# Performance work log

Measured on AMD Instinct MI355X. Metric: run time of the kernel, lower is better.

The kernel has to match this reference:

```python
import jax, jax.numpy as jnp
import numpy as np

B = 256
LSTM = 512
FEAT = 3 * 3 * 512 + 16 + 8  # 4632
N_ACT = 4
ACT_SHAPE = 64
NUM_STEPS = 20
CANVAS_IN = 6 * 32 * 32  # 6144
H1 = int(FEAT / (FEAT / LSTM) ** (1.0 / 3.0))  # 2223
H2 = int(FEAT / (FEAT / LSTM) ** (2.0 / 3.0))  # 1067


def setup_inputs() -> dict:
    key = jax.random.key(0)
    ks = jax.random.split(key, 32)

    def g(k, shape, scale=0.02):
        return jax.random.normal(k, shape, dtype=jnp.float32) * scale

    inp = {
        "actualCanvas": jax.random.normal(ks[0], (B, 3, 32, 32), dtype=jnp.float32),
        "objectiveCanvas": jax.random.normal(ks[1], (B, 3, 32, 32), dtype=jnp.float32),
        "last_action_end_position": jax.random.randint(ks[2], (B,), 0, ACT_SHAPE),
        "episode_percentage": jax.random.randint(ks[3], (B,), 0, NUM_STEPS),
        # feature extractor stub (flatten -> linear -> relu), output 4608
        "Wfe": g(ks[4], (4608, CANVAS_IN)), "bfe": jnp.zeros((4608,), jnp.float32),
        "emb_end": g(ks[5], (ACT_SHAPE, 16), 1.0),
        "emb_ep": g(ks[6], (NUM_STEPS, 8), 1.0),
        "W1": g(ks[7], (H1, FEAT)), "b1": jnp.zeros((H1,), jnp.float32),
        "W2": g(ks[8], (H2, H1)), "b2": jnp.zeros((H2,), jnp.float32),
        "W3": g(ks[9], (LSTM, H2)), "b3": jnp.zeros((LSTM,), jnp.float32),
        "W_ih": g(ks[10], (4 * LSTM, LSTM)), "W_hh": g(ks[11], (4 * LSTM, LSTM)),
        "b_ih": jnp.zeros((4 * LSTM,), jnp.float32), "b_hh": jnp.zeros((4 * LSTM,), jnp.float32),
        "Wd1": g(ks[12], (N_ACT, LSTM // 2, LSTM)), "bd1": jnp.zeros((N_ACT, LSTM // 2), jnp.float32),
        "Wd2": g(ks[13], (N_ACT, ACT_SHAPE, LSTM // 2)), "bd2": jnp.zeros((N_ACT, ACT_SHAPE), jnp.float32),
        "emb_dec": g(ks[14], (N_ACT, ACT_SHAPE, 16), 1.0),
        "Wout": g(ks[15], (LSTM, LSTM + 16)), "bout": jnp.zeros((LSTM,), jnp.float32),
    }
    return inp


def reference(actualCanvas, objectiveCanvas, last_action_end_position, episode_percentage,
              Wfe, bfe, emb_end, emb_ep, W1, b1, W2, b2, W3, b3,
              W_ih, W_hh, b_ih, b_hh, Wd1, bd1, Wd2, bd2, emb_dec, Wout, bout):
    # feature extractor on channel-concatenated canvases -> [B, 4608]
    x = jnp.concatenate([actualCanvas, objectiveCanvas], axis=1).reshape(B, -1)
    fv = jax.nn.relu(x @ Wfe.T + bfe)
    feats = jnp.concatenate([fv, emb_end[last_action_end_position], emb_ep[episode_percentage]], axis=1)
    # fc1->fc2->fc3 (dropout = eval mode / identity)
    h = jax.nn.relu(feats @ W1.T + b1)
    h = jax.nn.relu(h @ W2.T + b2)
    h = jax.nn.relu(h @ W3.T + b3)  # [B, LSTM]
    # single-step LSTM with zero initial state (first execution)
    gates = h @ W_ih.T + b_ih + b_hh  # h0 = 0 so recurrent matmul vanishes
    i, f, g_, o = jnp.split(gates, 4, axis=1)
    c = jax.nn.sigmoid(i) * jnp.tanh(g_)
    seed = jax.nn.sigmoid(o) * jnp.tanh(c)  # [B, LSTM]
    z = seed
    log_probabilities = jnp.zeros((B,), jnp.float32)
    entropy = jnp.float32(0.0)
    actions = []
    base_key = jax.random.key(42)
    for k in range(N_ACT):
        hm = jax.nn.relu(z @ Wd1[k].T + bd1[k])
        logits = hm @ Wd2[k].T + bd2[k]  # [B, ACT_SHAPE]
        logp = jax.nn.log_softmax(logits, axis=1)
        probs = jnp.exp(logp)
        entropy = entropy + jnp.sum(-probs * logp)
        act = jax.random.categorical(jax.random.fold_in(base_key, k), logits, axis=1)  # [B]
        actions.append(act)
        log_probabilities = log_probabilities + jnp.take_along_axis(logp, act[:, None], axis=1)[:, 0]
        emb_a = emb_dec[k][act]  # [B,16]
        z = jax.nn.relu(jnp.concatenate([z, emb_a], axis=1) @ Wout.T + bout)
    action = jnp.stack(actions, axis=1)  # [B, N_ACT]
    return action, entropy, log_probabilities
```

## Files before the change

### kernel.cpp

```cpp
#include <hip/hip_runtime.h>
#include <hip/hip_bf16.h>
#include <stdint.h>

#define B_SZ   256
#define LSTM_N 512
#define FEAT_N 4632
#define FV_N   4608
#define CIN_N  6144
#define HALF_CIN 3072
#define ACT_N  64
#define LDSW   72
#define LD_FEAT 4672
#define LD_ZEXT 576

typedef __attribute__((ext_vector_type(8))) short bf16x8;
typedef __attribute__((ext_vector_type(4))) float f32x4;

__device__ __forceinline__ short f2bf(float f) {
  uint32_t u = __float_as_uint(f);
  u += 0x7FFFu + ((u >> 16) & 1u);
  return (short)(u >> 16);
}
__device__ __forceinline__ float bf2f(short s) {
  return __uint_as_float(((uint32_t)(uint16_t)s) << 16);
}

__device__ __forceinline__ uint32_t rotl32(uint32_t x, int r) {
  return (x << r) | (x >> (32 - r));
}
__device__ __forceinline__ void threefry2x32(uint32_t k0, uint32_t k1,
                                             uint32_t x0, uint32_t x1,
                                             uint32_t& o0, uint32_t& o1) {
  uint32_t k2 = k0 ^ k1 ^ 0x1BD11BDAu;
  x0 += k0; x1 += k1;
  x0 += x1; x1 = rotl32(x1, 13); x1 ^= x0;
  x0 += x1; x1 = rotl32(x1, 15); x1 ^= x0;
  x0 += x1; x1 = rotl32(x1, 26); x1 ^= x0;
  x0 += x1; x1 = rotl32(x1,  6); x1 ^= x0;
  x0 += k1; x1 += k2 + 1u;
  x0 += x1; x1 = rotl32(x1, 17); x1 ^= x0;
  x0 += x1; x1 = rotl32(x1, 29); x1 ^= x0;
  x0 += x1; x1 = rotl32(x1, 16); x1 ^= x0;
  x0 += x1; x1 = rotl32(x1, 24); x1 ^= x0;
  x0 += k2; x1 += k0 + 2u;
  x0 += x1; x1 = rotl32(x1, 13); x1 ^= x0;
  x0 += x1; x1 = rotl32(x1, 15); x1 ^= x0;
  x0 += x1; x1 = rotl32(x1, 26); x1 ^= x0;
  x0 += x1; x1 = rotl32(x1,  6); x1 ^= x0;
  x0 += k0; x1 += k1 + 3u;
  x0 += x1; x1 = rotl32(x1, 17); x1 ^= x0;
  x0 += x1; x1 = rotl32(x1, 29); x1 ^= x0;
  x0 += x1; x1 = rotl32(x1, 16); x1 ^= x0;
  x0 += x1; x1 = rotl32(x1, 24); x1 ^= x0;
  x0 += k1; x1 += k2 + 4u;
  x0 += x1; x1 = rotl32(x1, 13); x1 ^= x0;
  x0 += x1; x1 = rotl32(x1, 15); x1 ^= x0;
  x0 += x1; x1 = rotl32(x1, 26); x1 ^= x0;
  x0 += x1; x1 = rotl32(x1,  6); x1 ^= x0;
  x0 += k2; x1 += k0 + 5u;
  o0 = x0; o1 = x1;
}

__global__ void concat_cvt_kernel(const float* __restrict__ act,
                                  const float* __restrict__ obj,
                                  short* __restrict__ xb) {
  int idx = blockIdx.x * 256 + threadIdx.x;
  if (idx >= B_SZ * 768) return;
  int row = idx / 768;
  int c8 = (idx - row * 768) * 8;
  const float* src = (c8 < HALF_CIN) ? (act + (size_t)row * HALF_CIN + c8)
                                     : (obj + (size_t)row * HALF_CIN + (c8 - HALF_CIN));
  float4 u = ((const float4*)src)[0];
  float4 v = ((const float4*)src)[1];
  bf16x8 r;
  r[0]=f2bf(u.x); r[1]=f2bf(u.y); r[2]=f2bf(u.z); r[3]=f2bf(u.w);
  r[4]=f2bf(v.x); r[5]=f2bf(v.y); r[6]=f2bf(v.z); r[7]=f2bf(v.w);
  *(bf16x8*)&xb[(size_t)row * CIN_N + c8] = r;
}

__global__ void fill_embs_kernel(const int* __restrict__ lastpos,
                                 const int* __restrict__ ep,
                                 const float* __restrict__ emb_end,
                                 const float* __restrict__ emb_ep,
                                 short* __restrict__ feats) {
  int b = blockIdx.x;
  int t = threadIdx.x;
  short* row = feats + (size_t)b * LD_FEAT;
  if (t < 16) {
    row[FV_N + t] = f2bf(emb_end[lastpos[b] * 16 + t]);
  } else if (t < 24) {
    row[FV_N + 16 + (t - 16)] = f2bf(emb_ep[ep[b] * 8 + (t - 16)]);
  } else {
    row[FV_N + t] = 0;
  }
}

__global__ __launch_bounds__(512) void gemm3_kernel(
    const short* __restrict__ A, int ldab,
    const float* __restrict__ W, int ldw,
    const float* __restrict__ bias1, const float* __restrict__ bias2,
    void* __restrict__ Cout, int ldc,
    short* __restrict__ P,
    int N, int K, int do_relu, int mode_f32, int kc, int nchunks) {
  __shared__ short Wlds[2][64 * LDSW];

  const int tid = threadIdx.x;
  const int w = tid >> 6, l = tid & 63, l15 = l & 15, lg = l >> 4;
  const int n0 = blockIdx.x * 64;
  const int Np = gridDim.x * 64;
  const int ks = blockIdx.y;
  const int kbeg = ks * kc;
  const int kend = (kbeg + kc < K) ? (kbeg + kc) : K;
  const int nk = (kend - kbeg + 63) >> 6;
  const bool wfast = ((ldw & 3) == 0);

  f32x4 acc[2][4];
#pragma unroll
  for (int i = 0; i < 2; ++i)
#pragma unroll
    for (int j = 0; j < 4; ++j) acc[i][j] = (f32x4){0.f, 0.f, 0.f, 0.f};

  const int wrow = tid >> 3, wq = tid & 7;

  auto loadW = [&](float4* dst, int k0) {
    int gn = n0 + wrow; if (gn >= N) gn = N - 1;
    int gk = k0 + (wq << 3);
    const float* p = W + (size_t)gn * ldw + gk;
    if (wfast && (k0 + 64 <= K)) {
      dst[0] = ((const float4*)p)[0];
      dst[1] = ((const float4*)p)[1];
    } else {
      float t[8];
#pragma unroll
      for (int j = 0; j < 8; ++j) t[j] = (gk + j < K) ? p[j] : 0.f;
      dst[0] = (float4){t[0], t[1], t[2], t[3]};
      dst[1] = (float4){t[4], t[5], t[6], t[7]};
    }
  };
  auto storeW = [&](const float4* src, int buf) {
    short4 s0, s1;
    s0.x = f2bf(src[0].x); s0.y = f2bf(src[0].y);
    s0.z = f2bf(src[0].z); s0.w = f2bf(src[0].w);
    s1.x = f2bf(src[1].x); s1.y = f2bf(src[1].y);
    s1.z = f2bf(src[1].z); s1.w = f2bf(src[1].w);
    short* q = &Wlds[buf][wrow * LDSW + (wq << 3)];
    *(short4*)q = s0;
    *(short4*)(q + 4) = s1;
  };
  auto loadA = [&](bf16x8* dst, int k0) {
#pragma unroll
    for (int mi = 0; mi < 2; ++mi)
#pragma unroll
      for (int kh = 0; kh < 2; ++kh) {
        int m = (w << 5) + (mi << 4) + l15;
        int kk = k0 + (kh << 5) + (lg << 3);
        dst[(mi << 1) + kh] = *(const bf16x8*)&A[(size_t)m * ldab + kk];
      }
  };

#define MFMA_STEP(ACUR, BUF)                                                        \
  {                                                                                 \
    _Pragma("unroll")                                                               \
    for (int nj = 0; nj < 4; ++nj) {                                                \
      const short* bp = &Wlds[BUF][((nj << 4) + l15) * LDSW + (lg << 3)];           \
      bf16x8 b0 = *(const bf16x8*)bp;                                               \
      bf16x8 b1 = *(const bf16x8*)(bp + 32);                                        \
      acc[0][nj] = __builtin_amdgcn_mfma_f32_16x16x32_bf16(ACUR[0], b0, acc[0][nj], 0, 0, 0); \
      acc[1][nj] = __builtin_amdgcn_mfma_f32_16x16x32_bf16(ACUR[2], b0, acc[1][nj], 0, 0, 0); \
      acc[0][nj] = __builtin_amdgcn_mfma_f32_16x16x32_bf16(ACUR[1], b1, acc[0][nj], 0, 0, 0); \
      acc[1][nj] = __builtin_amdgcn_mfma_f32_16x16x32_bf16(ACUR[3], b1, acc[1][nj], 0, 0, 0); \
    }                                                                               \
  }

#define STEP(KT, ACUR, ANXT, WCUR, WNXT, BUF, BUFN)          \
  {                                                          \
    if ((KT) + 1 < nk) loadA(ANXT, kbeg + (((KT) + 1) << 6));\
    if ((KT) + 2 < nk) loadW(WCUR, kbeg + (((KT) + 2) << 6));\
    MFMA_STEP(ACUR, BUF);                                    \
    if ((KT) + 1 < nk) { storeW(WNXT, BUFN); __syncthreads(); } \
  }

  bf16x8 a0[4], a1[4];
  float4 wr0[2], wr1[2];

  loadW(wr0, kbeg);
  loadA(a0, kbeg);
  storeW(wr0, 0);
  if (nk > 1) loadW(wr1, kbeg + 64);
  __syncthreads();

  for (int kt = 0; kt < nk; kt += 2) {
    STEP(kt, a0, a1, wr0, wr1, 0, 1);
    if (kt + 1 < nk) STEP(kt + 1, a1, a0, wr1, wr0, 1, 0);
  }

  if (nchunks == 1) {
#pragma unroll
    for (int nj = 0; nj < 4; ++nj) {
      int gn = n0 + (nj << 4) + l15;
      float bsum = 0.f;
      if (gn < N) {
        if (bias1) bsum += bias1[gn];
        if (bias2) bsum += bias2[gn];
      }
#pragma unroll
      for (int mi = 0; mi < 2; ++mi)
#pragma unroll
        for (int r = 0; r < 4; ++r) {
          int gm = (w << 5) + (mi << 4) + (lg << 2) + r;
          float v = (gn < N) ? (acc[mi][nj][r] + bsum) : 0.f;
          if (do_relu) v = fmaxf(v, 0.f);
          if (mode_f32) ((float*)Cout)[(size_t)gm * ldc + gn] = v;
          else          ((short*)Cout)[(size_t)gm * ldc + gn] = f2bf(v);
        }
    }
  } else {
    short* Pb = P + (size_t)ks * 256 * Np;
#pragma unroll
    for (int nj = 0; nj < 4; ++nj) {
      int gn = n0 + (nj << 4) + l15;
#pragma unroll
      for (int mi = 0; mi < 2; ++mi)
#pragma unroll
        for (int r = 0; r < 4; ++r) {
          int gm = (w << 5) + (mi << 4) + (lg << 2) + r;
          Pb[(size_t)gm * Np + gn] = f2bf(acc[mi][nj][r]);
        }
    }
  }
#undef STEP
#undef MFMA_STEP
}

__global__ void reduce_kernel(const short* __restrict__ P, int Np, int nchunks,
                              const float* __restrict__ bias1,
                              const float* __restrict__ bias2,
                              void* __restrict__ out, int ldc, int N,
                              int relu, int mode_f32) {
  int npack = Np >> 3;
  int idx = blockIdx.x * 256 + threadIdx.x;
  if (idx >= 256 * npack) return;
  int m = idx / npack;
  int n8 = (idx - m * npack) << 3;
  float s[8] = {0.f, 0.f, 0.f, 0.f, 0.f, 0.f, 0.f, 0.f};
  for (int ks = 0; ks < nchunks; ++ks) {
    bf16x8 v = *(const bf16x8*)&P[(size_t)ks * 256 * Np + (size_t)m * Np + n8];
#pragma unroll
    for (int j = 0; j < 8; ++j) s[j] += bf2f(v[j]);
  }
#pragma unroll
  for (int j = 0; j < 8; ++j) {
    int n = n8 + j;
    float r = 0.f;
    if (n < N) {
      r = s[j];
      if (bias1) r += bias1[n];
      if (bias2) r += bias2[n];
      if (relu) r = fmaxf(r, 0.f);
    }
    s[j] = r;
  }
  if (mode_f32) {
    float* o = (float*)out + (size_t)m * ldc + n8;
#pragma unroll
    for (int j = 0; j < 8; ++j) o[j] = s[j];
  } else {
    bf16x8 r;
#pragma unroll
    for (int j = 0; j < 8; ++j) r[j] = f2bf(s[j]);
    *(bf16x8*)((short*)out + (size_t)m * ldc + n8) = r;
  }
}

__global__ void lstm_kernel(const float* __restrict__ gates,
                            short* __restrict__ zext) {
  int idx = blockIdx.x * blockDim.x + threadIdx.x;
  if (idx >= B_SZ * LSTM_N) return;
  int b = idx >> 9;
  int n = idx & 511;
  const float* g = gates + (size_t)b * (4 * LSTM_N);
  float gi = g[n];
  float gg = g[2 * LSTM_N + n];
  float go = g[3 * LSTM_N + n];
  float si = 1.f / (1.f + expf(-gi));
  float so = 1.f / (1.f + expf(-go));
  float c = si * tanhf(gg);
  float h = so * tanhf(c);
  zext[(size_t)b * LD_ZEXT + n] = f2bf(h);
}

__global__ void sample_kernel(const float* __restrict__ logits,
                              const float* __restrict__ emb_dec_k,
                              short* __restrict__ zext,
                              int* __restrict__ act_out,
                              float* __restrict__ logp_out,
                              float* __restrict__ ent_out,
                              int k, int write_emb) {
  const int b = blockIdx.x;
  const int a = threadIdx.x;
  float logit = logits[b * ACT_N + a];

  float m = logit;
#pragma unroll
  for (int off = 32; off; off >>= 1) m = fmaxf(m, __shfl_xor(m, off));
  float e = expf(logit - m);
  float s = e;
#pragma unroll
  for (int off = 32; off; off >>= 1) s += __shfl_xor(s, off);
  float logp = logit - m - logf(s);

  float ent = -expf(logp) * logp;
#pragma unroll
  for (int off = 32; off; off >>= 1) ent += __shfl_xor(ent, off);

  uint32_t f0, f1;
  threefry2x32(0u, 42u, 0u, (uint32_t)k, f0, f1);
  uint32_t j = (uint32_t)(b * ACT_N + a);
  uint32_t o0, o1, bits;
  if (j < 8192u) {
    threefry2x32(f0, f1, j, j + 8192u, o0, o1);
    bits = o0;
  } else {
    threefry2x32(f0, f1, j - 8192u, j, o0, o1);
    bits = o1;
  }
  const float tiny = 1.17549435e-38f;
  float fu = __uint_as_float((bits >> 9) | 0x3f800000u) - 1.0f;
  float u = fmaxf(tiny, fu * (1.0f - tiny) + tiny);
  float gum = -logf(-logf(u));
  float pert = logit + gum;

  float bv = pert;
  int bi = a;
#pragma unroll
  for (int off = 32; off; off >>= 1) {
    float ov = __shfl_xor(bv, off);
    int oi = __shfl_xor(bi, off);
    if (ov > bv || (ov == bv && oi < bi)) { bv = ov; bi = oi; }
  }
  int act = bi;
  float lp_sel = __shfl(logp, act);

  if (a == 0) {
    act_out[b] = act;
    logp_out[b] = lp_sel;
    ent_out[b] = ent;
  }
  if (write_emb) {
    if (a < 16) zext[(size_t)b * LD_ZEXT + 512 + a] = f2bf(emb_dec_k[act * 16 + a]);
    else        zext[(size_t)b * LD_ZEXT + 512 + a] = 0;
  }
}

__global__ void finalize_kernel(const int* __restrict__ act,
                                const float* __restrict__ logp_k,
                                const float* __restrict__ ent,
                                float* __restrict__ out) {
  __shared__ float sred[4];
  int t = threadIdx.x;
#pragma unroll
  for (int k = 0; k < 4; ++k)
    out[t * 4 + k] = (float)act[k * 256 + t];
  float lp = 0.f;
#pragma unroll
  for (int k = 0; k < 4; ++k) lp += logp_k[k * 256 + t];
  out[1025 + t] = lp;

  float v = 0.f;
#pragma unroll
  for (int k = 0; k < 4; ++k) v += ent[k * 256 + t];
#pragma unroll
  for (int off = 32; off; off >>= 1) v += __shfl_xor(v, off);
  if ((t & 63) == 0) sred[t >> 6] = v;
  __syncthreads();
  if (t == 0) out[1024] = sred[0] + sred[1] + sred[2] + sred[3];
}

extern "C" void kernel_launch(void* const* d_in, const int* in_sizes, int n_in,
                              void* d_out, int out_size, void* d_ws, size_t ws_size,
                              hipStream_t stream) {
  float* out = (float*)d_out;
  char* out_bytes = (char*)d_out;
  auto sentinel = [&](int code) { hipMemsetAsync(out_bytes + 4096, code, 4, stream); };

  if (n_in < 25 || in_sizes[0] != B_SZ * 3 * 32 * 32 ||
      in_sizes[4] != FV_N * CIN_N || in_sizes[23] != LSTM_N * 528 ||
      in_sizes[9] <= 0 || in_sizes[9] > 8192 ||
      in_sizes[11] <= 0 || in_sizes[11] > 8192) {
    sentinel(0x42);
    return;
  }

  const float* actual = (const float*)d_in[0];
  const float* object = (const float*)d_in[1];
  const int* lastpos  = (const int*)d_in[2];
  const int* ep       = (const int*)d_in[3];
  const float* Wfe    = (const float*)d_in[4];
  const float* bfe    = (const float*)d_in[5];
  const float* emb_end= (const float*)d_in[6];
  const float* emb_ep = (const float*)d_in[7];
  const float* W1     = (const float*)d_in[8];
  const float* b1     = (const float*)d_in[9];
  const float* W2     = (const float*)d_in[10];
  const float* b2     = (const float*)d_in[11];
  const float* W3     = (const float*)d_in[12];
  const float* b3     = (const float*)d_in[13];
  const float* W_ih   = (const float*)d_in[14];
  const float* b_ih   = (const float*)d_in[16];
  const float* b_hh   = (const float*)d_in[17];
  const float* Wd1    = (const float*)d_in[18];
  const float* bd1    = (const float*)d_in[19];
  const float* Wd2    = (const float*)d_in[20];
  const float* bd2    = (const float*)d_in[21];
  const float* embdec = (const float*)d_in[22];
  const float* Wout   = (const float*)d_in[23];
  const float* bout   = (const float*)d_in[24];

  const int H1 = in_sizes[9];
  const int H2 = in_sizes[11];
  const int ldh1 = 64 * ((H1 + 63) / 64);
  const int ldh2 = 64 * ((H2 + 63) / 64);

  char* wsb = (char*)d_ws;
  size_t off = 0;
  auto alloc = [&](size_t bytes) {
    char* p = wsb + off;
    off += (bytes + 255) & ~(size_t)255;
    return p;
  };
  float* logpk = (float*)alloc(1024 * 4);
  float* entk  = (float*)alloc(1024 * 4);
  int*   actk  = (int*)alloc(1024 * 4);
  short* xb    = (short*)alloc((size_t)B_SZ * CIN_N * 2);
  short* feats = (short*)alloc((size_t)B_SZ * LD_FEAT * 2);
  short* h1    = (short*)alloc((size_t)B_SZ * ldh1 * 2);
  short* h2    = (short*)alloc((size_t)B_SZ * ldh2 * 2);
  short* h3    = (short*)alloc((size_t)B_SZ * 512 * 2);
  float* gates = (float*)alloc((size_t)B_SZ * 2048 * 4);
  short* zextA = (short*)alloc((size_t)B_SZ * LD_ZEXT * 2);
  short* zextB = (short*)alloc((size_t)B_SZ * LD_ZEXT * 2);
  short* hm    = (short*)alloc((size_t)B_SZ * 256 * 2);
  float* logit = (float*)alloc((size_t)B_SZ * 64 * 4);
  if (off + (1 << 20) > ws_size) {
    sentinel(0x43);
    return;
  }
  short* slab = (short*)(wsb + off);
  const size_t slab_bytes = ws_size - off;

  auto gemm = [&](const short* A, int ldab, const float* W, int ldw,
                  const float* bb1, const float* bb2,
                  void* C, int ldc, int N, int K, int relu, int mode_f32,
                  bool split) {
    int nblk = (N + 63) / 64;
    int Np = nblk * 64;
    int chunks = 1;
    int kc = 64 * ((K + 63) / 64);
    if (split) {
      int by_grid = (768 + nblk - 1) / nblk;
      int by_traffic = K / 320; if (by_traffic < 2) by_traffic = 2;
      int c = (by_grid < by_traffic) ? by_grid : by_traffic;
      int maxch = (K + 63) / 64; if (c > maxch) c = maxch;
      size_t cap = slab_bytes / ((size_t)256 * Np * 2);
      if ((size_t)c > cap) c = (int)cap;
      if (c < 1) c = 1;
      kc = 64 * ((K + 64 * c - 1) / (64 * c));
      chunks = (K + kc - 1) / kc;
    }
    dim3 g(nblk, chunks);
    gemm3_kernel<<<g, dim3(512), 0, stream>>>(
        A, ldab, W, ldw, bb1, bb2, C, ldc, slab, N, K, relu, mode_f32, kc, chunks);
    if (chunks > 1) {
      int npack = Np >> 3;
      reduce_kernel<<<dim3((256 * npack + 255) / 256), dim3(256), 0, stream>>>(
          slab, Np, chunks, bb1, bb2, C, ldc, N, relu, mode_f32);
    }
  };

  concat_cvt_kernel<<<dim3(768), dim3(256), 0, stream>>>(actual, object, xb);
  gemm(xb, CIN_N, Wfe, CIN_N, bfe, nullptr, feats, LD_FEAT, FV_N, CIN_N, 1, 0, true);
  fill_embs_kernel<<<dim3(B_SZ), dim3(64), 0, stream>>>(lastpos, ep, emb_end, emb_ep, feats);
  gemm(feats, LD_FEAT, W1, FEAT_N, b1, nullptr, h1, ldh1, H1, FEAT_N, 1, 0, true);
  gemm(h1, ldh1, W2, H1, b2, nullptr, h2, ldh2, H2, H1, 1, 0, true);
  gemm(h2, ldh2, W3, H2, b3, nullptr, h3, 512, LSTM_N, H2, 1, 0, true);
  gemm(h3, 512, W_ih, LSTM_N, b_ih, b_hh, gates, 2048, 4 * LSTM_N, LSTM_N, 0, 1, true);
  lstm_kernel<<<dim3((B_SZ * LSTM_N + 255) / 256), dim3(256), 0, stream>>>(gates, zextA);

  short* zcur = zextA;
  short* znxt = zextB;
  for (int k = 0; k < 4; ++k) {
    const float* Wd1k = Wd1 + (size_t)k * 256 * LSTM_N;
    const float* bd1k = bd1 + (size_t)k * 256;
    const float* Wd2k = Wd2 + (size_t)k * ACT_N * 256;
    const float* bd2k = bd2 + (size_t)k * ACT_N;
    const float* embk = embdec + (size_t)k * ACT_N * 16;
    gemm(zcur, LD_ZEXT, Wd1k, LSTM_N, bd1k, nullptr, hm, 256, 256, LSTM_N, 1, 0, false);
    gemm(hm, 256, Wd2k, 256, bd2k, nullptr, logit, 64, ACT_N, 256, 0, 1, false);
    sample_kernel<<<dim3(B_SZ), dim3(64), 0, stream>>>(
        logit, embk, zcur, actk + k * B_SZ, logpk + k * B_SZ,
        entk + k * B_SZ, k, (k < 3) ? 1 : 0);
    if (k < 3) {
      gemm(zcur, LD_ZEXT, Wout, 528, bout, nullptr, znxt, LD_ZEXT, LSTM_N, 528, 1, 0, false);
      short* t = zcur; zcur = znxt; znxt = t;
    }
  }

  finalize_kernel<<<dim3(1), dim3(256), 0, stream>>>(actk, logpk, entk, out);
}
```

Baseline: 313.6 us.

## Fuse LSTM gates into split-K reduce, fuse logits GEMM with sampling, deepen weight prefetch

```diff
diff --git a/kernel.cpp b/kernel.cpp
--- a/kernel.cpp
+++ b/kernel.cpp
@@ -78,6 +78,21 @@
   *(bf16x8*)&xb[(size_t)row * CIN_N + c8] = r;
 }
 
+__global__ void gumbel_kernel(float* __restrict__ gum) {
+  int idx = blockIdx.x * 256 + threadIdx.x;
+  if (idx >= 4 * 16384) return;
+  int k = idx >> 14;
+  uint32_t j = (uint32_t)(idx & 16383);
+  uint32_t f0, f1, o0, o1, bits;
+  threefry2x32(0u, 42u, 0u, (uint32_t)k, f0, f1);
+  if (j < 8192u) { threefry2x32(f0, f1, j, j + 8192u, o0, o1); bits = o0; }
+  else           { threefry2x32(f0, f1, j - 8192u, j, o0, o1); bits = o1; }
+  const float tiny = 1.17549435e-38f;
+  float fu = __uint_as_float((bits >> 9) | 0x3f800000u) - 1.0f;
+  float u = fmaxf(tiny, fu * (1.0f - tiny) + tiny);
+  gum[idx] = -logf(-logf(u));
+}
+
 __global__ void fill_embs_kernel(const int* __restrict__ lastpos,
                                  const int* __restrict__ ep,
                                  const float* __restrict__ emb_end,
@@ -86,13 +101,9 @@
   int b = blockIdx.x;
   int t = threadIdx.x;
   short* row = feats + (size_t)b * LD_FEAT;
-  if (t < 16) {
-    row[FV_N + t] = f2bf(emb_end[lastpos[b] * 16 + t]);
-  } else if (t < 24) {
-    row[FV_N + 16 + (t - 16)] = f2bf(emb_ep[ep[b] * 8 + (t - 16)]);
-  } else {
-    row[FV_N + t] = 0;
-  }
+  if (t < 16)      row[FV_N + t] = f2bf(emb_end[lastpos[b] * 16 + t]);
+  else if (t < 24) row[FV_N + 16 + (t - 16)] = f2bf(emb_ep[ep[b] * 8 + (t - 16)]);
+  else             row[FV_N + t] = 0;
 }
 
 __global__ __launch_bounds__(512) void gemm3_kernel(
@@ -121,6 +132,8 @@
     for (int j = 0; j < 4; ++j) acc[i][j] = (f32x4){0.f, 0.f, 0.f, 0.f};
 
   const int wrow = tid >> 3, wq = tid & 7;
+  float4 wrA[2], wrB[2], wrC[2], wrD[2];
+  bf16x8 a0[4], a1[4];
 
   auto loadW = [&](float4* dst, int k0) {
     int gn = n0 + wrow; if (gn >= N) gn = N - 1;
@@ -172,29 +185,32 @@
     }                                                                               \
   }
 
-#define STEP(KT, ACUR, ANXT, WCUR, WNXT, BUF, BUFN)          \
-  {                                                          \
-    if ((KT) + 1 < nk) loadA(ANXT, kbeg + (((KT) + 1) << 6));\
-    if ((KT) + 2 < nk) loadW(WCUR, kbeg + (((KT) + 2) << 6));\
-    MFMA_STEP(ACUR, BUF);                                    \
-    if ((KT) + 1 < nk) { storeW(WNXT, BUFN); __syncthreads(); } \
-  }
-
-  bf16x8 a0[4], a1[4];
-  float4 wr0[2], wr1[2];
-
-  loadW(wr0, kbeg);
+#define KSTEP(KT, WISS, WST, AC, AN, BUFC, BUFN)                      \
+  {                                                                   \
+    if ((KT) + 4 < nk) loadW(WISS, kbeg + (((KT) + 4) << 6));         \
+    if ((KT) + 1 < nk) loadA(AN, kbeg + (((KT) + 1) << 6));           \
+    MFMA_STEP(AC, BUFC);                                              \
+    if ((KT) + 1 < nk) { storeW(WST, BUFN); __syncthreads(); }        \
+  }
+
+  loadW(wrA, kbeg);
+  if (nk > 1) loadW(wrB, kbeg + 64);
+  if (nk > 2) loadW(wrC, kbeg + 128);
+  if (nk > 3) loadW(wrD, kbeg + 192);
   loadA(a0, kbeg);
-  storeW(wr0, 0);
-  if (nk > 1) loadW(wr1, kbeg + 64);
+  storeW(wrA, 0);
   __syncthreads();
 
-  for (int kt = 0; kt < nk; kt += 2) {
-    STEP(kt, a0, a1, wr0, wr1, 0, 1);
-    if (kt + 1 < nk) STEP(kt + 1, a1, a0, wr1, wr0, 1, 0);
-  }
-
-  if (nchunks == 1) {
+  for (int kt = 0; kt < nk; kt += 4) {
+    KSTEP(kt, wrA, wrB, a0, a1, 0, 1);
+    if (kt + 1 < nk) KSTEP(kt + 1, wrB, wrC, a1, a0, 1, 0);
+    if (kt + 2 < nk) KSTEP(kt + 2, wrC, wrD, a0, a1, 0, 1);
+    if (kt + 3 < nk) KSTEP(kt + 3, wrD, wrA, a1, a0, 1, 0);
+  }
+#undef KSTEP
+#undef MFMA_STEP
+
+  if (nchunks == 1 && Cout) {
 #pragma unroll
     for (int nj = 0; nj < 4; ++nj) {
       int gn = n0 + (nj << 4) + l15;
@@ -228,8 +244,6 @@
         }
     }
   }
-#undef STEP
-#undef MFMA_STEP
 }
 
 __global__ void reduce_kernel(const short* __restrict__ P, int Np, int nchunks,
@@ -272,83 +286,153 @@
   }
 }
 
-__global__ void lstm_kernel(const float* __restrict__ gates,
-                            short* __restrict__ zext) {
-  int idx = blockIdx.x * blockDim.x + threadIdx.x;
-  if (idx >= B_SZ * LSTM_N) return;
-  int b = idx >> 9;
-  int n = idx & 511;
-  const float* g = gates + (size_t)b * (4 * LSTM_N);
-  float gi = g[n];
-  float gg = g[2 * LSTM_N + n];
-  float go = g[3 * LSTM_N + n];
-  float si = 1.f / (1.f + expf(-gi));
-  float so = 1.f / (1.f + expf(-go));
-  float c = si * tanhf(gg);
-  float h = so * tanhf(c);
-  zext[(size_t)b * LD_ZEXT + n] = f2bf(h);
-}
-
-__global__ void sample_kernel(const float* __restrict__ logits,
-                              const float* __restrict__ emb_dec_k,
-                              short* __restrict__ zext,
-                              int* __restrict__ act_out,
-                              float* __restrict__ logp_out,
-                              float* __restrict__ ent_out,
-                              int k, int write_emb) {
-  const int b = blockIdx.x;
-  const int a = threadIdx.x;
-  float logit = logits[b * ACT_N + a];
-
-  float m = logit;
-#pragma unroll
-  for (int off = 32; off; off >>= 1) m = fmaxf(m, __shfl_xor(m, off));
-  float e = expf(logit - m);
-  float s = e;
-#pragma unroll
-  for (int off = 32; off; off >>= 1) s += __shfl_xor(s, off);
-  float logp = logit - m - logf(s);
-
-  float ent = -expf(logp) * logp;
-#pragma unroll
-  for (int off = 32; off; off >>= 1) ent += __shfl_xor(ent, off);
-
-  uint32_t f0, f1;
-  threefry2x32(0u, 42u, 0u, (uint32_t)k, f0, f1);
-  uint32_t j = (uint32_t)(b * ACT_N + a);
-  uint32_t o0, o1, bits;
-  if (j < 8192u) {
-    threefry2x32(f0, f1, j, j + 8192u, o0, o1);
-    bits = o0;
-  } else {
-    threefry2x32(f0, f1, j - 8192u, j, o0, o1);
-    bits = o1;
-  }
-  const float tiny = 1.17549435e-38f;
-  float fu = __uint_as_float((bits >> 9) | 0x3f800000u) - 1.0f;
-  float u = fmaxf(tiny, fu * (1.0f - tiny) + tiny);
-  float gum = -logf(-logf(u));
-  float pert = logit + gum;
-
-  float bv = pert;
-  int bi = a;
-#pragma unroll
-  for (int off = 32; off; off >>= 1) {
-    float ov = __shfl_xor(bv, off);
-    int oi = __shfl_xor(bi, off);
-    if (ov > bv || (ov == bv && oi < bi)) { bv = ov; bi = oi; }
-  }
-  int act = bi;
-  float lp_sel = __shfl(logp, act);
-
-  if (a == 0) {
-    act_out[b] = act;
-    logp_out[b] = lp_sel;
-    ent_out[b] = ent;
-  }
-  if (write_emb) {
-    if (a < 16) zext[(size_t)b * LD_ZEXT + 512 + a] = f2bf(emb_dec_k[act * 16 + a]);
-    else        zext[(size_t)b * LD_ZEXT + 512 + a] = 0;
+__global__ void reduce_lstm_kernel(const short* __restrict__ P, int nchunks,
+                                   const float* __restrict__ b_ih,
+                                   const float* __restrict__ b_hh,
+                                   short* __restrict__ zext) {
+  int idx = blockIdx.x * 256 + threadIdx.x;
+  if (idx >= 256 * 64) return;
+  int m = idx >> 6;
+  int n8 = (idx & 63) << 3;
+  float gi[8] = {}, gg[8] = {}, go[8] = {};
+  for (int ks = 0; ks < nchunks; ++ks) {
+    const short* base = P + ((size_t)ks * 256 + m) * 2048;
+    bf16x8 vi = *(const bf16x8*)(base + n8);
+    bf16x8 vg = *(const bf16x8*)(base + 1024 + n8);
+    bf16x8 vo = *(const bf16x8*)(base + 1536 + n8);
+#pragma unroll
+    for (int j = 0; j < 8; ++j) {
+      gi[j] += bf2f(vi[j]); gg[j] += bf2f(vg[j]); go[j] += bf2f(vo[j]);
+    }
+  }
+  bf16x8 hv;
+#pragma unroll
+  for (int j = 0; j < 8; ++j) {
+    int n = n8 + j;
+    float i_ = gi[j] + b_ih[n] + b_hh[n];
+    float g_ = gg[j] + b_ih[1024 + n] + b_hh[1024 + n];
+    float o_ = go[j] + b_ih[1536 + n] + b_hh[1536 + n];
+    float si = 1.f / (1.f + expf(-i_));
+    float so = 1.f / (1.f + expf(-o_));
+    float c = si * tanhf(g_);
+    hv[j] = f2bf(so * tanhf(c));
+  }
+  *(bf16x8*)&zext[(size_t)m * LD_ZEXT + n8] = hv;
+}
+
+__global__ __launch_bounds__(512) void logits_sample_kernel(
+    const short* __restrict__ hm,
+    const float* __restrict__ Wd2k,
+    const float* __restrict__ bd2k,
+    const float* __restrict__ gumk,
+    const float* __restrict__ embk,
+    short* __restrict__ zext,
+    int* __restrict__ act_out, float* __restrict__ logp_out,
+    float* __restrict__ ent_out, int write_emb) {
+  __shared__ short Wl[64 * 264];
+  const int tid = threadIdx.x;
+  const int w = tid >> 6, l = tid & 63, l15 = l & 15, lg = l >> 4;
+
+  {
+    int r = tid >> 3;
+    int c0 = (tid & 7) << 5;
+    const float* src = Wd2k + r * 256 + c0;
+    short* dst = &Wl[r * 264 + c0];
+#pragma unroll
+    for (int i = 0; i < 4; ++i) {
+      float4 u = ((const float4*)src)[2 * i];
+      float4 v = ((const float4*)src)[2 * i + 1];
+      bf16x8 t;
+      t[0]=f2bf(u.x); t[1]=f2bf(u.y); t[2]=f2bf(u.z); t[3]=f2bf(u.w);
+      t[4]=f2bf(v.x); t[5]=f2bf(v.y); t[6]=f2bf(v.z); t[7]=f2bf(v.w);
+      *(bf16x8*)(dst + 8 * i) = t;
+    }
+  }
+  __syncthreads();
+
+  f32x4 acc[2][4];
+#pragma unroll
+  for (int i = 0; i < 2; ++i)
+#pragma unroll
+    for (int j = 0; j < 4; ++j) acc[i][j] = (f32x4){0.f, 0.f, 0.f, 0.f};
+
+#pragma unroll
+  for (int kt = 0; kt < 4; ++kt) {
+    int k0 = kt << 6;
+    bf16x8 af[4];
+#pragma unroll
+    for (int mi = 0; mi < 2; ++mi)
+#pragma unroll
+      for (int kh = 0; kh < 2; ++kh) {
+        int m = (w << 5) + (mi << 4) + l15;
+        af[(mi << 1) + kh] = *(const bf16x8*)&hm[(size_t)m * 256 + k0 + (kh << 5) + (lg << 3)];
+      }
+#pragma unroll
+    for (int nj = 0; nj < 4; ++nj) {
+      const short* bp = &Wl[((nj << 4) + l15) * 264 + k0 + (lg << 3)];
+      bf16x8 b0 = *(const bf16x8*)bp;
+      bf16x8 b1 = *(const bf16x8*)(bp + 32);
+      acc[0][nj] = __builtin_amdgcn_mfma_f32_16x16x32_bf16(af[0], b0, acc[0][nj], 0, 0, 0);
+      acc[1][nj] = __builtin_amdgcn_mfma_f32_16x16x32_bf16(af[2], b0, acc[1][nj], 0, 0, 0);
+      acc[0][nj] = __builtin_amdgcn_mfma_f32_16x16x32_bf16(af[1], b1, acc[0][nj], 0, 0, 0);
+      acc[1][nj] = __builtin_amdgcn_mfma_f32_16x16x32_bf16(af[3], b1, acc[1][nj], 0, 0, 0);
+    }
+  }
+
+  float bcol[4];
+#pragma unroll
+  for (int nj = 0; nj < 4; ++nj) bcol[nj] = bd2k[(nj << 4) + l15];
+
+#pragma unroll
+  for (int mi = 0; mi < 2; ++mi) {
+#pragma unroll
+    for (int r = 0; r < 4; ++r) {
+      int row = (w << 5) + (mi << 4) + (lg << 2) + r;
+      float lv[4];
+#pragma unroll
+      for (int nj = 0; nj < 4; ++nj) lv[nj] = acc[mi][nj][r] + bcol[nj];
+      float mx = fmaxf(fmaxf(lv[0], lv[1]), fmaxf(lv[2], lv[3]));
+#pragma unroll
+      for (int off = 8; off; off >>= 1) mx = fmaxf(mx, __shfl_xor(mx, off));
+      float es = expf(lv[0]-mx) + expf(lv[1]-mx) + expf(lv[2]-mx) + expf(lv[3]-mx);
+#pragma unroll
+      for (int off = 8; off; off >>= 1) es += __shfl_xor(es, off);
+      float lse = logf(es);
+      float lp[4], ent = 0.f;
+#pragma unroll
+      for (int nj = 0; nj < 4; ++nj) {
+        lp[nj] = lv[nj] - mx - lse;
+        ent += -expf(lp[nj]) * lp[nj];
+      }
+#pragma unroll
+      for (int off = 8; off; off >>= 1) ent += __shfl_xor(ent, off);
+      float bv = -3.4e38f; int bc = 64; float blp = 0.f;
+#pragma unroll
+      for (int nj = 0; nj < 4; ++nj) {
+        int col = (nj << 4) + l15;
+        float pert = lv[nj] + gumk[row * 64 + col];
+        if (pert > bv || (pert == bv && col < bc)) { bv = pert; bc = col; blp = lp[nj]; }
+      }
+#pragma unroll
+      for (int off = 8; off; off >>= 1) {
+        float ov = __shfl_xor(bv, off);
+        int oc = __shfl_xor(bc, off);
+        float olp = __shfl_xor(blp, off);
+        if (ov > bv || (ov == bv && oc < bc)) { bv = ov; bc = oc; blp = olp; }
+      }
+      if (l15 == 0) {
+        act_out[row] = bc;
+        logp_out[row] = blp;
+        ent_out[row] = ent;
+      }
+      if (write_emb) {
+        short* zr = zext + (size_t)row * LD_ZEXT;
+        zr[512 + l15] = f2bf(embk[bc * 16 + l15]);
+        zr[528 + l15] = 0;
+        zr[544 + l15] = 0;
+        zr[560 + l15] = 0;
+      }
+    }
   }
 }
 
@@ -431,17 +515,16 @@
   float* logpk = (float*)alloc(1024 * 4);
   float* entk  = (float*)alloc(1024 * 4);
   int*   actk  = (int*)alloc(1024 * 4);
+  float* gumb  = (float*)alloc(4 * 16384 * 4);
   short* xb    = (short*)alloc((size_t)B_SZ * CIN_N * 2);
   short* feats = (short*)alloc((size_t)B_SZ * LD_FEAT * 2);
   short* h1    = (short*)alloc((size_t)B_SZ * ldh1 * 2);
   short* h2    = (short*)alloc((size_t)B_SZ * ldh2 * 2);
   short* h3    = (short*)alloc((size_t)B_SZ * 512 * 2);
-  float* gates = (float*)alloc((size_t)B_SZ * 2048 * 4);
   short* zextA = (short*)alloc((size_t)B_SZ * LD_ZEXT * 2);
   short* zextB = (short*)alloc((size_t)B_SZ * LD_ZEXT * 2);
   short* hm    = (short*)alloc((size_t)B_SZ * 256 * 2);
-  float* logit = (float*)alloc((size_t)B_SZ * 64 * 4);
-  if (off + (1 << 20) > ws_size) {
+  if (off + (4 << 20) > ws_size) {
     sentinel(0x43);
     return;
   }
@@ -451,16 +534,15 @@
   auto gemm = [&](const short* A, int ldab, const float* W, int ldw,
                   const float* bb1, const float* bb2,
                   void* C, int ldc, int N, int K, int relu, int mode_f32,
-                  bool split) {
+                  bool split, int fuse) {
     int nblk = (N + 63) / 64;
     int Np = nblk * 64;
     int chunks = 1;
     int kc = 64 * ((K + 63) / 64);
     if (split) {
-      int by_grid = (768 + nblk - 1) / nblk;
-      int by_traffic = K / 320; if (by_traffic < 2) by_traffic = 2;
-      int c = (by_grid < by_traffic) ? by_grid : by_traffic;
-      int maxch = (K + 63) / 64; if (c > maxch) c = maxch;
+      int c = (640 + nblk - 1) / nblk;
+      int capk = K >> 7; if (capk < 1) capk = 1;
+      if (c > capk) c = capk;
       size_t cap = slab_bytes / ((size_t)256 * Np * 2);
       if ((size_t)c > cap) c = (int)cap;
       if (c < 1) c = 1;
@@ -468,9 +550,13 @@
       chunks = (K + kc - 1) / kc;
     }
     dim3 g(nblk, chunks);
+    void* Ck = (fuse == 1) ? nullptr : C;
     gemm3_kernel<<<g, dim3(512), 0, stream>>>(
-        A, ldab, W, ldw, bb1, bb2, C, ldc, slab, N, K, relu, mode_f32, kc, chunks);
-    if (chunks > 1) {
+        A, ldab, W, ldw, bb1, bb2, Ck, ldc, slab, N, K, relu, mode_f32, kc, chunks);
+    if (fuse == 1) {
+      reduce_lstm_kernel<<<dim3(64), dim3(256), 0, stream>>>(
+          slab, chunks, bb1, bb2, (short*)C);
+    } else if (chunks > 1) {
       int npack = Np >> 3;
       reduce_kernel<<<dim3((256 * npack + 255) / 256), dim3(256), 0, stream>>>(
           slab, Np, chunks, bb1, bb2, C, ldc, N, relu, mode_f32);
@@ -478,13 +564,13 @@
   };
 
   concat_cvt_kernel<<<dim3(768), dim3(256), 0, stream>>>(actual, object, xb);
-  gemm(xb, CIN_N, Wfe, CIN_N, bfe, nullptr, feats, LD_FEAT, FV_N, CIN_N, 1, 0, true);
+  gumbel_kernel<<<dim3(256), dim3(256), 0, stream>>>(gumb);
+  gemm(xb, CIN_N, Wfe, CIN_N, bfe, nullptr, feats, LD_FEAT, FV_N, CIN_N, 1, 0, true, 0);
   fill_embs_kernel<<<dim3(B_SZ), dim3(64), 0, stream>>>(lastpos, ep, emb_end, emb_ep, feats);
-  gemm(feats, LD_FEAT, W1, FEAT_N, b1, nullptr, h1, ldh1, H1, FEAT_N, 1, 0, true);
-  gemm(h1, ldh1, W2, H1, b2, nullptr, h2, ldh2, H2, H1, 1, 0, true);
-  gemm(h2, ldh2, W3, H2, b3, nullptr, h3, 512, LSTM_N, H2, 1, 0, true);
-  gemm(h3, 512, W_ih, LSTM_N, b_ih, b_hh, gates, 2048, 4 * LSTM_N, LSTM_N, 0, 1, true);
-  lstm_kernel<<<dim3((B_SZ * LSTM_N + 255) / 256), dim3(256), 0, stream>>>(gates, zextA);
+  gemm(feats, LD_FEAT, W1, FEAT_N, b1, nullptr, h1, ldh1, H1, FEAT_N, 1, 0, true, 0);
+  gemm(h1, ldh1, W2, H1, b2, nullptr, h2, ldh2, H2, H1, 1, 0, true, 0);
+  gemm(h2, ldh2, W3, H2, b3, nullptr, h3, 512, LSTM_N, H2, 1, 0, true, 0);
+  gemm(h3, 512, W_ih, LSTM_N, b_ih, b_hh, zextA, LD_ZEXT, 4 * LSTM_N, LSTM_N, 0, 0, true, 1);
 
   short* zcur = zextA;
   short* znxt = zextB;
@@ -494,13 +580,12 @@
     const float* Wd2k = Wd2 + (size_t)k * ACT_N * 256;
     const float* bd2k = bd2 + (size_t)k * ACT_N;
     const float* embk = embdec + (size_t)k * ACT_N * 16;
-    gemm(zcur, LD_ZEXT, Wd1k, LSTM_N, bd1k, nullptr, hm, 256, 256, LSTM_N, 1, 0, false);
-    gemm(hm, 256, Wd2k, 256, bd2k, nullptr, logit, 64, ACT_N, 256, 0, 1, false);
-    sample_kernel<<<dim3(B_SZ), dim3(64), 0, stream>>>(
-        logit, embk, zcur, actk + k * B_SZ, logpk + k * B_SZ,
-        entk + k * B_SZ, k, (k < 3) ? 1 : 0);
+    gemm(zcur, LD_ZEXT, Wd1k, LSTM_N, bd1k, nullptr, hm, 256, 256, LSTM_N, 1, 0, false, 0);
+    logits_sample_kernel<<<dim3(1), dim3(512), 0, stream>>>(
+        hm, Wd2k, bd2k, gumb + k * 16384, embk, zcur,
+        actk + k * B_SZ, logpk + k * B_SZ, entk + k * B_SZ, (k < 3) ? 1 : 0);
     if (k < 3) {
-      gemm(zcur, LD_ZEXT, Wout, 528, bout, nullptr, znxt, LD_ZEXT, LSTM_N, 528, 1, 0, false);
+      gemm(zcur, LD_ZEXT, Wout, 528, bout, nullptr, znxt, LD_ZEXT, LSTM_N, 528, 1, 0, false, 0);
       short* t = zcur; zcur = znxt; znxt = t;
     }
   }
```

After: 358.4 us. 1.14x slower.
